# Optimization experiments

Measured on AMD Instinct MI355X. Metric: run time of the kernel, lower is better.

The kernel has to match this reference:

```python
import jax, jax.numpy as jnp
import numpy as np

TOP_K = 2

def setup_inputs() -> dict:
    key = jax.random.key(0)
    ks = jax.random.split(key, 8)
    B, S, H, E, F = 4, 2048, 1024, 8, 2048  # F = hidden * expansion(2)
    scale_in = 0.02
    return {
        "x": jax.random.normal(ks[0], (B, S, H), dtype=jnp.float32),
        "router_w": jax.random.normal(ks[1], (H, E), dtype=jnp.float32) * scale_in,
        "router_b": jnp.zeros((E,), dtype=jnp.float32),
        "w1": jax.random.normal(ks[2], (E, H, F), dtype=jnp.float32) * scale_in,
        "b1": jnp.zeros((E, F), dtype=jnp.float32),
        "w2": jax.random.normal(ks[3], (E, F, H), dtype=jnp.float32) * scale_in,
        "b2": jnp.zeros((E, H), dtype=jnp.float32),
    }

def reference(x, router_w, router_b, w1, b1, w2, b2):
    B, S, H = x.shape
    E = router_b.shape[0]
    T = B * S
    flat = x.reshape(T, H)
    # Router + top-k gating (softmax over the k selected logits, as in torch code)
    logits = flat @ router_w + router_b                       # [T, E]
    topk_scores, topk_idx = jax.lax.top_k(logits, TOP_K)      # [T, k]
    probs = jax.nn.softmax(topk_scores, axis=-1)              # [T, k]
    # Dense gate matrix: gates[t, e] = prob if e selected for token t else 0
    gates = jnp.zeros((T, E), dtype=flat.dtype).at[
        jnp.arange(T)[:, None], topk_idx
    ].add(probs)                                              # [T, E]
    # Expert FFNs computed as batched GEMMs over the expert axis
    h = jax.nn.relu(jnp.einsum('td,edf->etf', flat, w1) + b1[:, None, :])  # [E, T, F]
    eout = jnp.einsum('etf,efd->etd', h, w2) + b2[:, None, :]              # [E, T, H]
    out = jnp.einsum('etd,te->td', eout, gates)                            # [T, H]
    return out.reshape(B, S, H)
```

## Files before the change

kernel.cpp:

```cpp
#include <hip/hip_runtime.h>
#include <hip/hip_bf16.h>

#define T_TOK 8192
#define HDIM 1024
#define FDIM 2048
#define NEXP 8
#define NASSIGN (T_TOK * 2)
#define ROWCAP (NASSIGN + 256)
#define NHB 256
#define MAXT2 72

typedef __bf16 bf16;
typedef __bf16 bf16x4 __attribute__((ext_vector_type(4)));
typedef __bf16 bf16x8 __attribute__((ext_vector_type(8)));
typedef float f32x4 __attribute__((ext_vector_type(4)));

__device__ __forceinline__ void gload_lds16(const void* g, void* l) {
    __builtin_amdgcn_global_load_lds(
        (const __attribute__((address_space(1))) void*)(uintptr_t)g,
        (__attribute__((address_space(3))) void*)(uintptr_t)l,
        16, 0, 0);
}

__global__ __launch_bounds__(256) void transpose_to_bf16(
    const float* __restrict__ in, bf16* __restrict__ out, int R, int C) {
    __shared__ float tile[64][68];
    int e = blockIdx.z;
    const float* inp = in + (size_t)e * R * C;
    bf16* outp = out + (size_t)e * R * C;
    int c0 = blockIdx.x * 64, r0 = blockIdx.y * 64;
    int tid = threadIdx.x;
    int tx = tid & 15, ty = tid >> 4;
#pragma unroll
    for (int i = 0; i < 4; i++) {
        int row = ty + i * 16;
        float4 v = *(const float4*)&inp[(size_t)(r0 + row) * C + c0 + tx * 4];
        *(float4*)&tile[row][tx * 4] = v;
    }
    __syncthreads();
#pragma unroll
    for (int i = 0; i < 2; i++) {
        int idx = tid + i * 256;
        int c = idx >> 3, seg = idx & 7;
        bf16x8 v;
#pragma unroll
        for (int j = 0; j < 8; j++) v[j] = (bf16)tile[seg * 8 + j][c];
        *(bf16x8*)&outp[(size_t)(c0 + c) * R + r0 + seg * 8] = v;
    }
}

__global__ __launch_bounds__(256) void router_kernel(
    const float* __restrict__ x, const float* __restrict__ rw,
    const float* __restrict__ rb, int* __restrict__ expert_pair,
    float2* __restrict__ gate_pair, bf16* __restrict__ xb,
    int* __restrict__ hist) {
    __shared__ float rwT[NEXP][HDIM];
    __shared__ float rbs[NEXP];
    __shared__ int sh_pair[32];
    int tid = threadIdx.x;
    for (int i = tid; i < HDIM * NEXP / 4; i += 256) {
        float4 v = ((const float4*)rw)[i];
        int h = i >> 1, e0 = (i & 1) * 4;
        rwT[e0 + 0][h] = v.x;
        rwT[e0 + 1][h] = v.y;
        rwT[e0 + 2][h] = v.z;
        rwT[e0 + 3][h] = v.w;
    }
    if (tid < NEXP) rbs[tid] = rb[tid];
    __syncthreads();
    int wave = tid >> 6, lane = tid & 63;
    int tbase = blockIdx.x * 32 + wave * 8;

    for (int tk = 0; tk < 8; tk++) {
        int t = tbase + tk;
        const float4* xt = (const float4*)(x + (size_t)t * HDIM);
        float p[NEXP];
#pragma unroll
        for (int e = 0; e < NEXP; e++) p[e] = 0.f;
#pragma unroll
        for (int it = 0; it < 4; it++) {
            float4 v = xt[it * 64 + lane];
            bf16x4 bv = {(bf16)v.x, (bf16)v.y, (bf16)v.z, (bf16)v.w};
            *(bf16x4*)&xb[(size_t)t * HDIM + (it * 64 + lane) * 4] = bv;
            int h = (it * 64 + lane) * 4;
#pragma unroll
            for (int e = 0; e < NEXP; e++) {
                float4 wv = *(const float4*)&rwT[e][h];
                p[e] += v.x * wv.x + v.y * wv.y + v.z * wv.z + v.w * wv.w;
            }
        }
#pragma unroll
        for (int off = 32; off >= 1; off >>= 1) {
#pragma unroll
            for (int e = 0; e < NEXP; e++) p[e] += __shfl_xor(p[e], off, 64);
        }
        if (lane == 0) {
            float lg[NEXP];
#pragma unroll
            for (int e = 0; e < NEXP; e++) lg[e] = p[e] + rbs[e];
            int e0 = 0;
#pragma unroll
            for (int e = 1; e < NEXP; e++)
                if (lg[e] > lg[e0]) e0 = e;
            int e1 = -1;
#pragma unroll
            for (int e = 0; e < NEXP; e++) {
                if (e == e0) continue;
                if (e1 < 0 || lg[e] > lg[e1]) e1 = e;
            }
            float z = expf(lg[e1] - lg[e0]);
            int pair = e0 | (e1 << 16);
            expert_pair[t] = pair;
            sh_pair[wave * 8 + tk] = pair;
            gate_pair[t] = make_float2(1.f / (1.f + z), z / (1.f + z));
        }
    }
    __syncthreads();
    if (wave == 0) {
        int tl = lane >> 1, j = lane & 1;
        int e = (sh_pair[tl] >> (16 * j)) & 0xffff;
#pragma unroll
        for (int ee = 0; ee < NEXP; ee++) {
            unsigned long long m = __ballot(e == ee);
            if (lane == ee) hist[blockIdx.x * NEXP + ee] = __popcll(m);
        }
    }
}

__global__ __launch_bounds__(256) void scan_kernel(
    const int* __restrict__ hist, int* __restrict__ start,
    int* __restrict__ cnt, int* __restrict__ offs,
    int* __restrict__ tile_e2, int* __restrict__ tile_m2,
    int* __restrict__ ntiles2) {
    __shared__ int h[NHB * NEXP];
    __shared__ int tot[NEXP];
    __shared__ int offsh[NEXP];
    int tid = threadIdx.x;
    for (int i = tid; i < NHB * NEXP; i += 256) h[i] = hist[i];
    __syncthreads();
    if (tid < NEXP) {
        int s = 0;
        for (int b = 0; b < NHB; b++) s += h[b * NEXP + tid];
        tot[tid] = s;
        cnt[tid] = s;
    }
    __syncthreads();
    if (tid == 0) {
        int o = 0;
        for (int e = 0; e < NEXP; e++) {
            offsh[e] = o;
            offs[e] = o;
            o += tot[e];
        }
        int idx2 = 0;
        for (int e = 0; e < NEXP; e++) {
            int nt = (tot[e] + 255) >> 8;
            for (int m = 0; m < nt; m++) {
                tile_e2[idx2] = e;
                tile_m2[idx2] = m;
                idx2++;
            }
        }
        ntiles2[0] = idx2;
    }
    __syncthreads();
    if (tid < NEXP) {
        int run = offsh[tid];
        for (int b = 0; b < NHB; b++) {
            start[b * NEXP + tid] = run;
            run += h[b * NEXP + tid];
        }
    }
}

__global__ __launch_bounds__(64) void scatter_kernel(
    const int* __restrict__ expert_pair, const float2* __restrict__ gate_pair,
    const int* __restrict__ start, int* __restrict__ perm,
    float* __restrict__ gatebuf, int* __restrict__ rowbuf) {
    int lane = threadIdx.x;
    int a = blockIdx.x * 64 + lane;
    int t = a >> 1, j = a & 1;
    int e = (expert_pair[t] >> (16 * j)) & 0xffff;
    float2 gp = gate_pair[t];
    float g = j ? gp.y : gp.x;
    int rank = 0;
    unsigned long long below = (1ull << lane) - 1ull;
#pragma unroll
    for (int ee = 0; ee < NEXP; ee++) {
        unsigned long long m = __ballot(e == ee);
        if (ee == e) rank = __popcll(m & below);
    }
    int pos = start[blockIdx.x * NEXP + e] + rank;
    perm[pos] = t;
    gatebuf[pos] = g;
    rowbuf[a] = pos;
}

template <bool RELU, bool GATE, bool GATHER, int K, int N>
__global__ __launch_bounds__(512, 4) void moe_gemm_p(
    const bf16* __restrict__ A, const bf16* __restrict__ B,
    const float* __restrict__ bias, const float* __restrict__ gates,
    bf16* __restrict__ out, const int* __restrict__ cnt,
    const int* __restrict__ offs, const int* __restrict__ tile_e2,
    const int* __restrict__ tile_m2, const int* __restrict__ ntiles2,
    const int* __restrict__ perm) {
    constexpr int NT = N / 128;
    constexpr int nk = K / 32;
    int ntl = ntiles2[0];
    int nact = ntl * NT;
    int f = blockIdx.x;
    if (f >= nact) return;
    int q8 = nact >> 3, r8 = nact & 7;
    int xcd = f & 7, rest = f >> 3;
    int wg = (xcd < r8) ? (xcd * (q8 + 1) + rest)
                        : (r8 * (q8 + 1) + (xcd - r8) * q8 + rest);
    int tile = wg / NT, ncol = wg - tile * NT;
    int e = tile_e2[tile];
    int n_cnt = cnt[e];
    int off_e = offs[e];
    int m0 = tile_m2[tile] * 256;
    int n0 = ncol * 128;

    __shared__ bf16 As[3][256][32];
    __shared__ bf16 Bs[3][128][32];

    int tid = threadIdx.x;
    int lane = tid & 63;
    int wave = tid >> 6;
    int wm = wave & 1;
    int wn = wave >> 1;
    int quad = lane >> 4, l16 = lane & 15;
    int rsw = (quad ^ ((l16 >> 1) & 3)) * 8;

    const bf16* Be = B + (size_t)e * (size_t)N * K;

    int r0s = tid >> 2;
    int segs = (tid & 3) ^ ((tid >> 3) & 3);
    const bf16* agA0;
    const bf16* agA1;
    if (GATHER) {
        int g0 = off_e + m0 + r0s;
        int g1 = off_e + m0 + 128 + r0s;
        g0 = g0 < NASSIGN ? g0 : NASSIGN - 1;
        g1 = g1 < NASSIGN ? g1 : NASSIGN - 1;
        agA0 = A + (size_t)perm[g0] * K + segs * 8;
        agA1 = A + (size_t)perm[g1] * K + segs * 8;
    } else {
        const bf16* Ae = A + (size_t)off_e * K;
        agA0 = Ae + (size_t)(m0 + r0s) * K + segs * 8;
        agA1 = Ae + (size_t)(m0 + 128 + r0s) * K + segs * 8;
    }
    const bf16* bgB0 = Be + (size_t)(n0 + r0s) * K + segs * 8;

    auto STG = [&](int buf, int kt) {
        bf16* Ab = (bf16*)As + (size_t)buf * (256 * 32);
        bf16* Bb = (bf16*)Bs + (size_t)buf * (128 * 32);
        gload_lds16(agA0 + (size_t)kt * 32, Ab + (wave * 64) * 8);
        gload_lds16(agA1 + (size_t)kt * 32, Ab + (512 + wave * 64) * 8);
        gload_lds16(bgB0 + (size_t)kt * 32, Bb + (wave * 64) * 8);
    };

    f32x4 acc[8][2];
#pragma unroll
    for (int i = 0; i < 8; i++)
#pragma unroll
        for (int j = 0; j < 2; j++) acc[i][j] = f32x4{0.f, 0.f, 0.f, 0.f};

    STG(0, 0);
    STG(1, 1);

    int b = 0, bs = 2;
    for (int t = 0; t < nk; t++) {
        if (t + 2 < nk) {
            STG(bs, t + 2);
            asm volatile("s_waitcnt vmcnt(6)" ::: "memory");
        } else if (t + 2 == nk) {
            asm volatile("s_waitcnt vmcnt(3)" ::: "memory");
        } else {
            asm volatile("s_waitcnt vmcnt(0)" ::: "memory");
        }
        asm volatile("s_barrier" ::: "memory");

        const bf16* Ab = (const bf16*)As + (size_t)b * (256 * 32);
        const bf16* Bb = (const bf16*)Bs + (size_t)b * (128 * 32);
        bf16x8 bf0 = *(const bf16x8*)(Bb + (wn * 32 + 0 * 16 + l16) * 32 + rsw);
        bf16x8 bf1 = *(const bf16x8*)(Bb + (wn * 32 + 1 * 16 + l16) * 32 + rsw);
        bf16x8 af[4];
#pragma unroll
        for (int mi = 0; mi < 4; mi++)
            af[mi] = *(const bf16x8*)(Ab + (wm * 128 + mi * 16 + l16) * 32 + rsw);
        asm volatile("s_waitcnt lgkmcnt(0)" ::: "memory");
        __builtin_amdgcn_s_setprio(1);
#pragma unroll
        for (int mi = 0; mi < 4; mi++) {
            acc[mi][0] = __builtin_amdgcn_mfma_f32_16x16x32_bf16(af[mi], bf0, acc[mi][0], 0, 0, 0);
            acc[mi][1] = __builtin_amdgcn_mfma_f32_16x16x32_bf16(af[mi], bf1, acc[mi][1], 0, 0, 0);
        }
        __builtin_amdgcn_s_setprio(0);
#pragma unroll
        for (int mi = 0; mi < 4; mi++)
            af[mi] = *(const bf16x8*)(Ab + (wm * 128 + (4 + mi) * 16 + l16) * 32 + rsw);
        asm volatile("s_waitcnt lgkmcnt(0)" ::: "memory");
        __builtin_amdgcn_s_setprio(1);
#pragma unroll
        for (int mi = 0; mi < 4; mi++) {
            acc[4 + mi][0] = __builtin_amdgcn_mfma_f32_16x16x32_bf16(af[mi], bf0, acc[4 + mi][0], 0, 0, 0);
            acc[4 + mi][1] = __builtin_amdgcn_mfma_f32_16x16x32_bf16(af[mi], bf1, acc[4 + mi][1], 0, 0, 0);
        }
        __builtin_amdgcn_s_setprio(0);
        asm volatile("s_barrier" ::: "memory");

        b = (b == 2) ? 0 : b + 1;
        bs = (bs == 2) ? 0 : bs + 1;
    }

#pragma unroll
    for (int mi = 0; mi < 8; mi++)
#pragma unroll
        for (int nj = 0; nj < 2; nj++)
#pragma unroll
            for (int r = 0; r < 4; r++) {
                int m = m0 + wm * 128 + mi * 16 + quad * 4 + r;
                if (m < n_cnt) {
                    int n = n0 + wn * 32 + nj * 16 + l16;
                    float v = acc[mi][nj][r] + bias[e * N + n];
                    if (RELU) v = v > 0.f ? v : 0.f;
                    if (GATE) v *= gates[off_e + m];
                    out[(size_t)(off_e + m) * N + n] = (bf16)v;
                }
            }
}

__global__ __launch_bounds__(256) void combine_kernel(
    const bf16* __restrict__ eout, const int* __restrict__ rowbuf,
    float* __restrict__ out) {
    int c = blockIdx.x * 256 + threadIdx.x;
    int t = c >> 7;
    int n = (c & 127) * 8;
    int r0 = rowbuf[2 * t], r1 = rowbuf[2 * t + 1];
    const bf16* p0 = eout + (size_t)r0 * HDIM + n;
    const bf16* p1 = eout + (size_t)r1 * HDIM + n;
    bf16x8 a = *(const bf16x8*)p0;
    bf16x8 b = *(const bf16x8*)p1;
    float* o = out + (size_t)t * HDIM + n;
    float4 v0 = {(float)a[0] + (float)b[0], (float)a[1] + (float)b[1],
                 (float)a[2] + (float)b[2], (float)a[3] + (float)b[3]};
    float4 v1 = {(float)a[4] + (float)b[4], (float)a[5] + (float)b[5],
                 (float)a[6] + (float)b[6], (float)a[7] + (float)b[7]};
    *(float4*)o = v0;
    *(float4*)(o + 4) = v1;
}

extern "C" void kernel_launch(void* const* d_in, const int* in_sizes, int n_in,
                              void* d_out, int out_size, void* d_ws, size_t ws_size,
                              hipStream_t stream) {
    const float* x = (const float*)d_in[0];
    const float* rw = (const float*)d_in[1];
    const float* rb = (const float*)d_in[2];
    const float* w1 = (const float*)d_in[3];
    const float* b1 = (const float*)d_in[4];
    const float* w2 = (const float*)d_in[5];
    const float* b2 = (const float*)d_in[6];
    float* out = (float*)d_out;

    char* ws = (char*)d_ws;
    size_t o = 0;
    auto alloc = [&](size_t bytes) {
        char* p = ws + o;
        o += (bytes + 255) & ~(size_t)255;
        return p;
    };
    bf16* w1t = (bf16*)alloc((size_t)NEXP * FDIM * HDIM * 2);
    bf16* w2t = (bf16*)alloc((size_t)NEXP * HDIM * FDIM * 2);
    bf16* hbuf = (bf16*)alloc((size_t)ROWCAP * FDIM * 2);
    bf16* eout = (bf16*)alloc((size_t)ROWCAP * HDIM * 2);
    bf16* xb = (bf16*)alloc((size_t)T_TOK * HDIM * 2);
    int* expert_pair = (int*)alloc((size_t)T_TOK * 4);
    float2* gate_pair = (float2*)alloc((size_t)T_TOK * 8);
    int* hist = (int*)alloc((size_t)NHB * NEXP * 4);
    int* start = (int*)alloc((size_t)NHB * NEXP * 4);
    int* perm = (int*)alloc((size_t)NASSIGN * 4);
    float* gatebuf = (float*)alloc((size_t)NASSIGN * 4);
    int* rowbuf = (int*)alloc((size_t)NASSIGN * 4);
    int* cnt = (int*)alloc(256);
    int* offs = (int*)alloc(256);
    int* tile_e2 = (int*)alloc((size_t)MAXT2 * 4);
    int* tile_m2 = (int*)alloc((size_t)MAXT2 * 4);
    int* ntiles2 = (int*)alloc(256);

    transpose_to_bf16<<<dim3(FDIM / 64, HDIM / 64, NEXP), 256, 0, stream>>>(w1, w1t, HDIM, FDIM);
    transpose_to_bf16<<<dim3(HDIM / 64, FDIM / 64, NEXP), 256, 0, stream>>>(w2, w2t, FDIM, HDIM);
    router_kernel<<<NHB, 256, 0, stream>>>(x, rw, rb, expert_pair, gate_pair, xb, hist);
    scan_kernel<<<1, 256, 0, stream>>>(hist, start, cnt, offs, tile_e2, tile_m2, ntiles2);
    scatter_kernel<<<NHB, 64, 0, stream>>>(expert_pair, gate_pair, start, perm, gatebuf, rowbuf);
    moe_gemm_p<true, false, true, HDIM, FDIM><<<dim3(MAXT2 * (FDIM / 128)), 512, 0, stream>>>(
        xb, w1t, b1, nullptr, hbuf, cnt, offs, tile_e2, tile_m2, ntiles2, perm);
    moe_gemm_p<false, true, false, FDIM, HDIM><<<dim3(MAXT2 * (HDIM / 128)), 512, 0, stream>>>(
        hbuf, w2t, b2, gatebuf, eout, cnt, offs, tile_e2, tile_m2, ntiles2, nullptr);
    combine_kernel<<<T_TOK * HDIM / 8 / 256, 256, 0, stream>>>(eout, rowbuf, out);
}
```

Measured before the change: 449.1 us.

## Fuse combine into second expert GEMM via atomic scatter-add; merge weight transposes

The second expert GEMM now scales each row by its gate and atomically adds it in fp32 directly into the zero-initialised output at the token index, replacing the bf16 eout buffer and the separate combine kernel. The two weight transposes are merged into one launch, and an XOR swizzle is added to the LDS tile to reduce bank conflicts. The change removes one kernel and an eout round trip but adds a zeroing pass and many scattered fp32 atomics whose contention and throughput may offset the savings.

```diff
diff --git a/kernel.cpp b/kernel.cpp
--- a/kernel.cpp
+++ b/kernel.cpp
@@ -22,20 +22,42 @@
         16, 0, 0);
 }
 
-__global__ __launch_bounds__(256) void transpose_to_bf16(
-    const float* __restrict__ in, bf16* __restrict__ out, int R, int C) {
+__global__ __launch_bounds__(256) void zero_kernel(float4* __restrict__ p) {
+    p[(size_t)blockIdx.x * 256 + threadIdx.x] = float4{0.f, 0.f, 0.f, 0.f};
+}
+
+__global__ __launch_bounds__(256) void transpose_both_bf16(
+    const float* __restrict__ w1, bf16* __restrict__ w1t,
+    const float* __restrict__ w2, bf16* __restrict__ w2t) {
     __shared__ float tile[64][68];
     int e = blockIdx.z;
-    const float* inp = in + (size_t)e * R * C;
-    bf16* outp = out + (size_t)e * R * C;
-    int c0 = blockIdx.x * 64, r0 = blockIdx.y * 64;
+    int bx = blockIdx.x;
+    const float* inp;
+    bf16* outp;
+    int R, C, c0, r0;
+    if (bx < 512) {
+        R = HDIM;
+        C = FDIM;
+        inp = w1 + (size_t)e * R * C;
+        outp = w1t + (size_t)e * R * C;
+        c0 = (bx & 31) * 64;
+        r0 = (bx >> 5) * 64;
+    } else {
+        int b = bx - 512;
+        R = FDIM;
+        C = HDIM;
+        inp = w2 + (size_t)e * R * C;
+        outp = w2t + (size_t)e * R * C;
+        c0 = (b & 15) * 64;
+        r0 = (b >> 4) * 64;
+    }
     int tid = threadIdx.x;
     int tx = tid & 15, ty = tid >> 4;
 #pragma unroll
     for (int i = 0; i < 4; i++) {
         int row = ty + i * 16;
         float4 v = *(const float4*)&inp[(size_t)(r0 + row) * C + c0 + tx * 4];
-        *(float4*)&tile[row][tx * 4] = v;
+        *(float4*)&tile[row][(tx * 4) ^ ((row >> 3) << 2)] = v;
     }
     __syncthreads();
 #pragma unroll
@@ -44,7 +66,8 @@
         int c = idx >> 3, seg = idx & 7;
         bf16x8 v;
 #pragma unroll
-        for (int j = 0; j < 8; j++) v[j] = (bf16)tile[seg * 8 + j][c];
+        for (int j = 0; j < 8; j++)
+            v[j] = (bf16)tile[seg * 8 + j][c ^ (seg << 2)];
         *(bf16x8*)&outp[(size_t)(c0 + c) * R + r0 + seg * 8] = v;
     }
 }
@@ -176,7 +199,7 @@
 __global__ __launch_bounds__(64) void scatter_kernel(
     const int* __restrict__ expert_pair, const float2* __restrict__ gate_pair,
     const int* __restrict__ start, int* __restrict__ perm,
-    float* __restrict__ gatebuf, int* __restrict__ rowbuf) {
+    float* __restrict__ gatebuf) {
     int lane = threadIdx.x;
     int a = blockIdx.x * 64 + lane;
     int t = a >> 1, j = a & 1;
@@ -193,17 +216,16 @@
     int pos = start[blockIdx.x * NEXP + e] + rank;
     perm[pos] = t;
     gatebuf[pos] = g;
-    rowbuf[a] = pos;
-}
-
-template <bool RELU, bool GATE, bool GATHER, int K, int N>
+}
+
+template <bool RELU, bool GATE, bool GATHER, bool ATOMIC, int K, int N>
 __global__ __launch_bounds__(512, 4) void moe_gemm_p(
     const bf16* __restrict__ A, const bf16* __restrict__ B,
     const float* __restrict__ bias, const float* __restrict__ gates,
-    bf16* __restrict__ out, const int* __restrict__ cnt,
-    const int* __restrict__ offs, const int* __restrict__ tile_e2,
-    const int* __restrict__ tile_m2, const int* __restrict__ ntiles2,
-    const int* __restrict__ perm) {
+    bf16* __restrict__ out, float* __restrict__ fout,
+    const int* __restrict__ cnt, const int* __restrict__ offs,
+    const int* __restrict__ tile_e2, const int* __restrict__ tile_m2,
+    const int* __restrict__ ntiles2, const int* __restrict__ perm) {
     constexpr int NT = N / 128;
     constexpr int nk = K / 32;
     int ntl = ntiles2[0];
@@ -317,38 +339,30 @@
 #pragma unroll
     for (int mi = 0; mi < 8; mi++)
 #pragma unroll
-        for (int nj = 0; nj < 2; nj++)
-#pragma unroll
-            for (int r = 0; r < 4; r++) {
-                int m = m0 + wm * 128 + mi * 16 + quad * 4 + r;
-                if (m < n_cnt) {
-                    int n = n0 + wn * 32 + nj * 16 + l16;
-                    float v = acc[mi][nj][r] + bias[e * N + n];
-                    if (RELU) v = v > 0.f ? v : 0.f;
-                    if (GATE) v *= gates[off_e + m];
-                    out[(size_t)(off_e + m) * N + n] = (bf16)v;
+        for (int r = 0; r < 4; r++) {
+            int m = m0 + wm * 128 + mi * 16 + quad * 4 + r;
+            if (m < n_cnt) {
+                if (ATOMIC) {
+                    int tok = perm[off_e + m];
+                    float g = gates[off_e + m];
+#pragma unroll
+                    for (int nj = 0; nj < 2; nj++) {
+                        int n = n0 + wn * 32 + nj * 16 + l16;
+                        float v = (acc[mi][nj][r] + bias[e * N + n]) * g;
+                        atomicAdd(&fout[(size_t)tok * N + n], v);
+                    }
+                } else {
+#pragma unroll
+                    for (int nj = 0; nj < 2; nj++) {
+                        int n = n0 + wn * 32 + nj * 16 + l16;
+                        float v = acc[mi][nj][r] + bias[e * N + n];
+                        if (RELU) v = v > 0.f ? v : 0.f;
+                        if (GATE) v *= gates[off_e + m];
+                        out[(size_t)(off_e + m) * N + n] = (bf16)v;
+                    }
                 }
             }
-}
-
-__global__ __launch_bounds__(256) void combine_kernel(
-    const bf16* __restrict__ eout, const int* __restrict__ rowbuf,
-    float* __restrict__ out) {
-    int c = blockIdx.x * 256 + threadIdx.x;
-    int t = c >> 7;
-    int n = (c & 127) * 8;
-    int r0 = rowbuf[2 * t], r1 = rowbuf[2 * t + 1];
-    const bf16* p0 = eout + (size_t)r0 * HDIM + n;
-    const bf16* p1 = eout + (size_t)r1 * HDIM + n;
-    bf16x8 a = *(const bf16x8*)p0;
-    bf16x8 b = *(const bf16x8*)p1;
-    float* o = out + (size_t)t * HDIM + n;
-    float4 v0 = {(float)a[0] + (float)b[0], (float)a[1] + (float)b[1],
-                 (float)a[2] + (float)b[2], (float)a[3] + (float)b[3]};
-    float4 v1 = {(float)a[4] + (float)b[4], (float)a[5] + (float)b[5],
-                 (float)a[6] + (float)b[6], (float)a[7] + (float)b[7]};
-    *(float4*)o = v0;
-    *(float4*)(o + 4) = v1;
+        }
 }
 
 extern "C" void kernel_launch(void* const* d_in, const int* in_sizes, int n_in,
@@ -373,7 +387,6 @@
     bf16* w1t = (bf16*)alloc((size_t)NEXP * FDIM * HDIM * 2);
     bf16* w2t = (bf16*)alloc((size_t)NEXP * HDIM * FDIM * 2);
     bf16* hbuf = (bf16*)alloc((size_t)ROWCAP * FDIM * 2);
-    bf16* eout = (bf16*)alloc((size_t)ROWCAP * HDIM * 2);
     bf16* xb = (bf16*)alloc((size_t)T_TOK * HDIM * 2);
     int* expert_pair = (int*)alloc((size_t)T_TOK * 4);
     float2* gate_pair = (float2*)alloc((size_t)T_TOK * 8);
@@ -381,21 +394,24 @@
     int* start = (int*)alloc((size_t)NHB * NEXP * 4);
     int* perm = (int*)alloc((size_t)NASSIGN * 4);
     float* gatebuf = (float*)alloc((size_t)NASSIGN * 4);
-    int* rowbuf = (int*)alloc((size_t)NASSIGN * 4);
     int* cnt = (int*)alloc(256);
     int* offs = (int*)alloc(256);
     int* tile_e2 = (int*)alloc((size_t)MAXT2 * 4);
     int* tile_m2 = (int*)alloc((size_t)MAXT2 * 4);
     int* ntiles2 = (int*)alloc(256);
 
-    transpose_to_bf16<<<dim3(FDIM / 64, HDIM / 64, NEXP), 256, 0, stream>>>(w1, w1t, HDIM, FDIM);
-    transpose_to_bf16<<<dim3(HDIM / 64, FDIM / 64, NEXP), 256, 0, stream>>>(w2, w2t, FDIM, HDIM);
+    zero_kernel<<<T_TOK * HDIM / 4 / 256, 256, 0, stream>>>((float4*)out);
+
+    transpose_both_bf16<<<dim3(1024, 1, NEXP), 256, 0, stream>>>(w1, w1t, w2, w2t);
     router_kernel<<<NHB, 256, 0, stream>>>(x, rw, rb, expert_pair, gate_pair, xb, hist);
     scan_kernel<<<1, 256, 0, stream>>>(hist, start, cnt, offs, tile_e2, tile_m2, ntiles2);
-    scatter_kernel<<<NHB, 64, 0, stream>>>(expert_pair, gate_pair, start, perm, gatebuf, rowbuf);
-    moe_gemm_p<true, false, true, HDIM, FDIM><<<dim3(MAXT2 * (FDIM / 128)), 512, 0, stream>>>(
-        xb, w1t, b1, nullptr, hbuf, cnt, offs, tile_e2, tile_m2, ntiles2, perm);
-    moe_gemm_p<false, true, false, FDIM, HDIM><<<dim3(MAXT2 * (HDIM / 128)), 512, 0, stream>>>(
-        hbuf, w2t, b2, gatebuf, eout, cnt, offs, tile_e2, tile_m2, ntiles2, nullptr);
-    combine_kernel<<<T_TOK * HDIM / 8 / 256, 256, 0, stream>>>(eout, rowbuf, out);
-}
+    scatter_kernel<<<NHB, 64, 0, stream>>>(expert_pair, gate_pair, start, perm, gatebuf);
+    moe_gemm_p<true, false, true, false, HDIM, FDIM>
+        <<<dim3(MAXT2 * (FDIM / 128)), 512, 0, stream>>>(
+            xb, w1t, b1, nullptr, hbuf, nullptr, cnt, offs, tile_e2, tile_m2,
+            ntiles2, perm);
+    moe_gemm_p<false, true, false, true, FDIM, HDIM>
+        <<<dim3(MAXT2 * (HDIM / 128)), 512, 0, stream>>>(
+            hbuf, w2t, b2, gatebuf, nullptr, out, cnt, offs, tile_e2, tile_m2,
+            ntiles2, perm);
+}
```

New measurement: 487.0 us. 8.5% more time.
